# Optimization experiments

Hardware: AMD Instinct MI355X
Metric: run time of the kernel (lower is better)

## Reference

```python
import jax, jax.numpy as jnp
import numpy as np

N = 100000
E = 3200000
H_MLP = 30   # EdgeMLP hidden dim
H_GCN = 10   # GCNEvaluator hidden dim
D_IN = 6     # node_dim + token_dim


def setup_inputs() -> dict:
    key = jax.random.key(0)
    ks = jax.random.split(key, 24)
    s = 0.1
    inp = {
        "x": jax.random.normal(ks[0], (N, 1), jnp.float32),
        "token": jax.random.normal(ks[1], (N, 5), jnp.float32),
        "edge_attr_gen": jax.random.normal(ks[2], (E, 1), jnp.float32),
        "edge_attr_eval": jax.random.uniform(ks[3], (E, 2), jnp.float32),
        "gumbel": jax.random.gumbel(ks[4], (E, 2), jnp.float32),
        "edge_index": jax.random.randint(ks[5], (2, E), 0, N, jnp.int32),
        # EdgeMLP params: Linear(13,30), Linear(30,30), Linear(30,30), Linear(30,2)
        "W0": jax.random.normal(ks[6], (2 * D_IN + 1, H_MLP), jnp.float32) * s,
        "b0": jnp.zeros((H_MLP,), jnp.float32),
        "W1": jax.random.normal(ks[7], (H_MLP, H_MLP), jnp.float32) * s,
        "b1": jnp.zeros((H_MLP,), jnp.float32),
        "W2": jax.random.normal(ks[8], (H_MLP, H_MLP), jnp.float32) * s,
        "b2": jnp.zeros((H_MLP,), jnp.float32),
        "W3": jax.random.normal(ks[9], (H_MLP, 2), jnp.float32) * s,
        "b3": jnp.zeros((2,), jnp.float32),
        # GCNEvaluator params
        "Wl": jax.random.normal(ks[10], (1, 1), jnp.float32) * s,   # edge_weight_lin
        "bl": jnp.zeros((1,), jnp.float32),
        "Wc": jax.random.normal(ks[11], (D_IN, H_GCN), jnp.float32) * s,  # GCNConv weight
        "bc": jnp.zeros((H_GCN,), jnp.float32),
        "Wo": jax.random.normal(ks[12], (H_GCN, 1), jnp.float32) * s,     # output Linear
        "bo": jnp.zeros((1,), jnp.float32),
    }
    return inp


def reference(x, token, edge_attr_gen, edge_attr_eval, gumbel, edge_index,
              W0, b0, W1, b1, W2, b2, W3, b3, Wl, bl, Wc, bc, Wo, bo):
    src = edge_index[0]
    tgt = edge_index[1]
    x_all = jnp.concatenate([x, token], axis=-1)              # [N, 6]

    # ---- generate_graph: edge gather + concat + MLP ----
    ef = jnp.concatenate([x_all[src], x_all[tgt], edge_attr_gen], axis=-1)  # [E, 13]
    h = jax.nn.relu(ef @ W0 + b0)
    h = jax.nn.relu(h @ W1 + b1)
    h = jax.nn.relu(h @ W2 + b2)
    logits = h @ W3 + b3                                      # [E, 2]

    # gumbel_softmax(tau=1.0, hard=True) with straight-through
    y_soft = jax.nn.softmax(logits + gumbel, axis=-1)
    y_hard = jax.nn.one_hot(jnp.argmax(y_soft, axis=-1), 2, dtype=y_soft.dtype)
    y = y_hard + y_soft - jax.lax.stop_gradient(y_soft)
    edge_value = y[:, 1:2]                                    # [E, 1]

    # ---- evaluate_graph: GCNEvaluator ----
    combined = jnp.concatenate([edge_attr_eval, edge_value], axis=-1)  # [E, 3]
    mask = combined[:, -2] * (1.0 - combined[:, -1])
    ew = jax.nn.sigmoid((combined[:, :1] @ Wl + bl)[:, 0]) * mask      # [E]

    # GCNConv(add_self_loops=True, normalize=True)
    loop = jnp.arange(N, dtype=src.dtype)
    row = jnp.concatenate([src, loop])
    col = jnp.concatenate([tgt, loop])
    w = jnp.concatenate([ew, jnp.ones((N,), ew.dtype)])
    deg = jax.ops.segment_sum(w, col, num_segments=N)
    dis = jnp.where(deg > 0, jax.lax.rsqrt(jnp.where(deg > 0, deg, 1.0)), 0.0)
    norm = dis[row] * w * dis[col]
    xw = x_all @ Wc                                            # [N, 10]
    agg = jax.ops.segment_sum(norm[:, None] * xw[row], col, num_segments=N) + bc
    out = jax.nn.sigmoid(agg @ Wo + bo)                        # [N, 1]
    return out
```

## Files before the change

kernel.cpp:

```cpp
#include <hip/hip_runtime.h>

#define NN 100000
#define NE 3200000
#define HM 30
#define HG 10
#define MAXK 26
#define OVF_CAP 8192

__global__ __launch_bounds__(256) void wtrans_kernel(
    const float* __restrict__ W0, const float* __restrict__ W1,
    const float* __restrict__ W2,
    float* __restrict__ W0T, float* __restrict__ W1T, float* __restrict__ W2T)
{
    for (int idx = threadIdx.x; idx < HM * 13; idx += 256) {
        int j = idx / 13, i = idx % 13;
        W0T[j * 16 + i] = W0[i * HM + j];
    }
    for (int idx = threadIdx.x; idx < HM * HM; idx += 256) {
        int j = idx / HM, i = idx % HM;
        W1T[j * 32 + i] = W1[i * HM + j];
        W2T[j * 32 + i] = W2[i * HM + j];
    }
}

__global__ __launch_bounds__(256) void pack_kernel(
    const float* __restrict__ x, const float* __restrict__ token,
    const float* __restrict__ Wc,
    float* __restrict__ xall8, float* __restrict__ xwp)
{
    __shared__ float sWc[6 * HG];
    if (threadIdx.x < 6 * HG) sWc[threadIdx.x] = Wc[threadIdx.x];
    __syncthreads();

    int n = blockIdx.x * 256 + threadIdx.x;
    if (n >= NN) return;

    float xa[6];
    xa[0] = x[n];
    #pragma unroll
    for (int i = 0; i < 5; i++) xa[1 + i] = token[n * 5 + i];

    float4* x4 = (float4*)xall8;
    x4[n * 2 + 0] = make_float4(xa[0], xa[1], xa[2], xa[3]);
    x4[n * 2 + 1] = make_float4(xa[4], xa[5], 0.f, 0.f);

    float w[12];
    #pragma unroll
    for (int k = 0; k < HG; k++) {
        float a = 0.f;
        #pragma unroll
        for (int i = 0; i < 6; i++) a = fmaf(xa[i], sWc[i * HG + k], a);
        w[k] = a;
    }
    w[10] = 0.f; w[11] = 0.f;
    float4* wp = (float4*)(xwp + (size_t)n * 12);
    wp[0] = make_float4(w[0], w[1], w[2], w[3]);
    wp[1] = make_float4(w[4], w[5], w[6], w[7]);
    wp[2] = make_float4(w[8], w[9], w[10], w[11]);
}

__global__ __launch_bounds__(256) void edge_mlp5_kernel(
    const float* __restrict__ xall8,
    const float* __restrict__ eg, const float* __restrict__ ee,
    const float* __restrict__ gum, const int* __restrict__ eidx,
    const float* __restrict__ W0T, const float* __restrict__ b0,
    const float* __restrict__ W1T, const float* __restrict__ b1,
    const float* __restrict__ W2T, const float* __restrict__ b2,
    const float* __restrict__ W3, const float* __restrict__ b3,
    const float* __restrict__ Wl, const float* __restrict__ bl,
    float2* __restrict__ slots, int* __restrict__ cnt,
    int* __restrict__ ohead, int* __restrict__ onxt,
    float* __restrict__ ovf_w, int* __restrict__ ovf_s, int* __restrict__ novf)
{
    int e = blockIdx.x * 256 + threadIdx.x;
    int s = eidx[e];
    int t = eidx[NE + e];

    const float4* x4 = (const float4*)xall8;
    float4 qa = x4[s * 2], qb = x4[s * 2 + 1];
    float4 qc = x4[t * 2], qd = x4[t * 2 + 1];
    float ef[13] = { qa.x, qa.y, qa.z, qa.w, qb.x, qb.y,
                     qc.x, qc.y, qc.z, qc.w, qd.x, qd.y, eg[e] };

    float h[HM], g[HM];
    #pragma unroll
    for (int j = 0; j < HM; j++) {
        float a = b0[j];
        #pragma unroll
        for (int i = 0; i < 13; i++) a = fmaf(ef[i], W0T[j * 16 + i], a);
        h[j] = fmaxf(a, 0.f);
    }
    #pragma unroll
    for (int j = 0; j < HM; j++) {
        float a = b1[j];
        #pragma unroll
        for (int i = 0; i < HM; i++) a = fmaf(h[i], W1T[j * 32 + i], a);
        g[j] = fmaxf(a, 0.f);
    }
    #pragma unroll
    for (int j = 0; j < HM; j++) {
        float a = b2[j];
        #pragma unroll
        for (int i = 0; i < HM; i++) a = fmaf(g[i], W2T[j * 32 + i], a);
        h[j] = fmaxf(a, 0.f);
    }

    float l0 = b3[0], l1 = b3[1];
    #pragma unroll
    for (int i = 0; i < HM; i++) {
        l0 = fmaf(h[i], W3[i * 2 + 0], l0);
        l1 = fmaf(h[i], W3[i * 2 + 1], l1);
    }

    const float2 g2 = ((const float2*)gum)[e];
    float v0 = l0 + g2.x;
    float v1 = l1 + g2.y;

    float ew = 0.f;
    if (!(v1 > v0)) {
        const float2 e2 = ((const float2*)ee)[e];
        float z = fmaf(e2.x, Wl[0], bl[0]);
        ew = e2.y / (1.f + __expf(-z));
    }
    if (ew != 0.f) {
        int slot = atomicAdd(&cnt[t], 1);
        if (slot < MAXK) {
            slots[(size_t)t * MAXK + slot] = make_float2(ew, __int_as_float(s));
        } else {
            int i = atomicAdd(novf, 1);
            if (i < OVF_CAP) {
                ovf_w[i] = ew;
                ovf_s[i] = s;
                onxt[i] = atomicExch(&ohead[t], i);
            }
        }
    }
}

__global__ __launch_bounds__(256) void node_deg_kernel(
    const float2* __restrict__ slots, const int* __restrict__ cnt,
    const int* __restrict__ ohead, const int* __restrict__ onxt,
    const float* __restrict__ ovf_w,
    float* __restrict__ xwp, float* __restrict__ dis)
{
    int n = blockIdx.x * 256 + threadIdx.x;
    if (n >= NN) return;

    int c = cnt[n];
    int cc = c < MAXK ? c : MAXK;
    float deg = 0.f;
    for (int j = 0; j < cc; j++) deg += slots[(size_t)n * MAXK + j].x;
    for (int i = ohead[n]; i >= 0; i = onxt[i]) deg += ovf_w[i];

    float d = rsqrtf(deg + 1.0f);
    dis[n] = d;

    float4* wp = (float4*)(xwp + (size_t)n * 12);
    #pragma unroll
    for (int q = 0; q < 3; q++) {
        float4 v = wp[q];
        v.x *= d; v.y *= d; v.z *= d; v.w *= d;
        wp[q] = v;
    }
}

__global__ __launch_bounds__(256) void gather_out2_kernel(
    const float2* __restrict__ slots, const int* __restrict__ cnt,
    const int* __restrict__ ohead, const int* __restrict__ onxt,
    const float* __restrict__ ovf_w, const int* __restrict__ ovf_s,
    const float* __restrict__ z, const float* __restrict__ dis,
    const float* __restrict__ bc, const float* __restrict__ Wo,
    const float* __restrict__ bo, float* __restrict__ out)
{
    __shared__ float sbc[12], sWo[12], sbo;
    if (threadIdx.x < 12) {
        sbc[threadIdx.x] = (threadIdx.x < HG) ? bc[threadIdx.x] : 0.f;
        sWo[threadIdx.x] = (threadIdx.x < HG) ? Wo[threadIdx.x] : 0.f;
    }
    if (threadIdx.x == 0) sbo = bo[0];
    __syncthreads();

    int n = blockIdx.x * 256 + threadIdx.x;
    if (n >= NN) return;

    const float4* Z = (const float4*)z;
    float4 A0 = make_float4(0.f, 0.f, 0.f, 0.f), A1 = A0, A2 = A0;

    int c = cnt[n];
    int cc = c < MAXK ? c : MAXK;
    for (int j = 0; j < cc; j++) {
        float2 p = slots[(size_t)n * MAXK + j];
        float w = p.x;
        int s = __float_as_int(p.y);
        float4 z0 = Z[s * 3], z1 = Z[s * 3 + 1], z2 = Z[s * 3 + 2];
        A0.x = fmaf(w, z0.x, A0.x); A0.y = fmaf(w, z0.y, A0.y);
        A0.z = fmaf(w, z0.z, A0.z); A0.w = fmaf(w, z0.w, A0.w);
        A1.x = fmaf(w, z1.x, A1.x); A1.y = fmaf(w, z1.y, A1.y);
        A1.z = fmaf(w, z1.z, A1.z); A1.w = fmaf(w, z1.w, A1.w);
        A2.x = fmaf(w, z2.x, A2.x); A2.y = fmaf(w, z2.y, A2.y);
    }
    for (int i = ohead[n]; i >= 0; i = onxt[i]) {
        float w = ovf_w[i];
        int s = ovf_s[i];
        float4 z0 = Z[s * 3], z1 = Z[s * 3 + 1], z2 = Z[s * 3 + 2];
        A0.x = fmaf(w, z0.x, A0.x); A0.y = fmaf(w, z0.y, A0.y);
        A0.z = fmaf(w, z0.z, A0.z); A0.w = fmaf(w, z0.w, A0.w);
        A1.x = fmaf(w, z1.x, A1.x); A1.y = fmaf(w, z1.y, A1.y);
        A1.z = fmaf(w, z1.z, A1.z); A1.w = fmaf(w, z1.w, A1.w);
        A2.x = fmaf(w, z2.x, A2.x); A2.y = fmaf(w, z2.y, A2.y);
    }

    float4 s0 = Z[n * 3], s1 = Z[n * 3 + 1], s2 = Z[n * 3 + 2];
    A0.x += s0.x; A0.y += s0.y; A0.z += s0.z; A0.w += s0.w;
    A1.x += s1.x; A1.y += s1.y; A1.z += s1.z; A1.w += s1.w;
    A2.x += s2.x; A2.y += s2.y;

    float d = dis[n];
    float v[10] = { A0.x, A0.y, A0.z, A0.w, A1.x, A1.y, A1.z, A1.w, A2.x, A2.y };
    float o = sbo;
    #pragma unroll
    for (int k = 0; k < HG; k++)
        o = fmaf(fmaf(v[k], d, sbc[k]), sWo[k], o);
    out[n] = 1.f / (1.f + __expf(-o));
}

__global__ __launch_bounds__(256) void edge_mlp_kernel(
    const float* __restrict__ x, const float* __restrict__ token,
    const float* __restrict__ eg, const float* __restrict__ ee,
    const float* __restrict__ gum, const int* __restrict__ eidx,
    const float* __restrict__ W0, const float* __restrict__ b0,
    const float* __restrict__ W1, const float* __restrict__ b1,
    const float* __restrict__ W2, const float* __restrict__ b2,
    const float* __restrict__ W3, const float* __restrict__ b3,
    const float* __restrict__ Wl, const float* __restrict__ bl,
    float* __restrict__ ew_out, float* __restrict__ deg)
{
    __shared__ float sW0[13 * HM];
    __shared__ float sW1[HM * HM];
    __shared__ float sW2[HM * HM];
    __shared__ float sW3f[HM * 2];
    __shared__ float sb0[HM], sb1[HM], sb2[HM], sb3[2];
    __shared__ float sWl, sbl;

    for (int i = threadIdx.x; i < 13 * HM; i += 256) sW0[i] = W0[i];
    for (int i = threadIdx.x; i < HM * HM; i += 256) sW1[i] = W1[i];
    for (int i = threadIdx.x; i < HM * HM; i += 256) sW2[i] = W2[i];
    for (int i = threadIdx.x; i < HM * 2; i += 256) sW3f[i] = W3[i];
    if (threadIdx.x < HM) {
        sb0[threadIdx.x] = b0[threadIdx.x];
        sb1[threadIdx.x] = b1[threadIdx.x];
        sb2[threadIdx.x] = b2[threadIdx.x];
    }
    if (threadIdx.x < 2) sb3[threadIdx.x] = b3[threadIdx.x];
    if (threadIdx.x == 0) { sWl = Wl[0]; sbl = bl[0]; }
    __syncthreads();

    int e = blockIdx.x * 256 + threadIdx.x;
    if (e >= NE) return;
    int s = eidx[e];
    int t = eidx[NE + e];

    float ef[13];
    ef[0] = x[s];
    #pragma unroll
    for (int i = 0; i < 5; i++) ef[1 + i] = token[s * 5 + i];
    ef[6] = x[t];
    #pragma unroll
    for (int i = 0; i < 5; i++) ef[7 + i] = token[t * 5 + i];
    ef[12] = eg[e];

    float h[HM], h2[HM];
    #pragma unroll
    for (int j = 0; j < HM; j++) {
        float a = sb0[j];
        #pragma unroll
        for (int i = 0; i < 13; i++) a = fmaf(ef[i], sW0[i * HM + j], a);
        h[j] = a > 0.f ? a : 0.f;
    }
    #pragma unroll
    for (int j = 0; j < HM; j++) {
        float a = sb1[j];
        #pragma unroll
        for (int i = 0; i < HM; i++) a = fmaf(h[i], sW1[i * HM + j], a);
        h2[j] = a > 0.f ? a : 0.f;
    }
    #pragma unroll
    for (int j = 0; j < HM; j++) {
        float a = sb2[j];
        #pragma unroll
        for (int i = 0; i < HM; i++) a = fmaf(h2[i], sW2[i * HM + j], a);
        h[j] = a > 0.f ? a : 0.f;
    }
    float l0 = sb3[0], l1 = sb3[1];
    #pragma unroll
    for (int i = 0; i < HM; i++) {
        l0 = fmaf(h[i], sW3f[i * 2 + 0], l0);
        l1 = fmaf(h[i], sW3f[i * 2 + 1], l1);
    }
    const float2 g2 = ((const float2*)gum)[e];
    float v0 = l0 + g2.x, v1 = l1 + g2.y;
    float ew = 0.f;
    if (!(v1 > v0)) {
        const float2 ee2 = ((const float2*)ee)[e];
        float z = fmaf(ee2.x, sWl, sbl);
        ew = ee2.y / (1.f + __expf(-z));
    }
    ew_out[e] = ew;
    if (ew != 0.f) atomicAdd(&deg[t], ew);
}

__global__ __launch_bounds__(256) void node_pre_kernel(
    const float* __restrict__ x, const float* __restrict__ token,
    const float* __restrict__ Wc, const float* __restrict__ deg,
    float* __restrict__ xw, float* __restrict__ dis)
{
    __shared__ float sWc[6 * HG];
    if (threadIdx.x < 6 * HG) sWc[threadIdx.x] = Wc[threadIdx.x];
    __syncthreads();
    int n = blockIdx.x * 256 + threadIdx.x;
    if (n >= NN) return;
    float xa[6];
    xa[0] = x[n];
    #pragma unroll
    for (int i = 0; i < 5; i++) xa[1 + i] = token[n * 5 + i];
    #pragma unroll
    for (int k = 0; k < HG; k++) {
        float a = 0.f;
        #pragma unroll
        for (int i = 0; i < 6; i++) a = fmaf(xa[i], sWc[i * HG + k], a);
        xw[n * HG + k] = a;
    }
    dis[n] = rsqrtf(deg[n] + 1.0f);
}

__global__ __launch_bounds__(256) void edge_scatter_kernel(
    const int* __restrict__ eidx, const float* __restrict__ ew,
    const float* __restrict__ dis, const float* __restrict__ xw,
    float* __restrict__ agg)
{
    int e = blockIdx.x * 256 + threadIdx.x;
    if (e >= NE) return;
    float w = ew[e];
    if (w == 0.f) return;
    int s = eidx[e];
    int t = eidx[NE + e];
    float norm = dis[s] * w * dis[t];
    #pragma unroll
    for (int k = 0; k < HG; k++)
        atomicAdd(&agg[t * HG + k], norm * xw[s * HG + k]);
}

__global__ __launch_bounds__(256) void node_out_kernel(
    const float* __restrict__ agg, const float* __restrict__ xw,
    const float* __restrict__ dis, const float* __restrict__ bc,
    const float* __restrict__ Wo, const float* __restrict__ bo,
    float* __restrict__ out)
{
    __shared__ float sbc[HG], sWo[HG], sbo;
    if (threadIdx.x < HG) { sbc[threadIdx.x] = bc[threadIdx.x]; sWo[threadIdx.x] = Wo[threadIdx.x]; }
    if (threadIdx.x == 0) sbo = bo[0];
    __syncthreads();
    int n = blockIdx.x * 256 + threadIdx.x;
    if (n >= NN) return;
    float d = dis[n];
    float self = d * d;
    float acc = sbo;
    #pragma unroll
    for (int k = 0; k < HG; k++) {
        float v = agg[n * HG + k] + xw[n * HG + k] * self + sbc[k];
        acc = fmaf(v, sWo[k], acc);
    }
    out[n] = 1.f / (1.f + __expf(-acc));
}

extern "C" void kernel_launch(void* const* d_in, const int* in_sizes, int n_in,
                              void* d_out, int out_size, void* d_ws, size_t ws_size,
                              hipStream_t stream) {
    const float* x   = (const float*)d_in[0];
    const float* tok = (const float*)d_in[1];
    const float* eg  = (const float*)d_in[2];
    const float* ee  = (const float*)d_in[3];
    const float* gum = (const float*)d_in[4];
    const int*   ei  = (const int*)d_in[5];
    const float* W0  = (const float*)d_in[6];
    const float* b0  = (const float*)d_in[7];
    const float* W1  = (const float*)d_in[8];
    const float* b1  = (const float*)d_in[9];
    const float* W2  = (const float*)d_in[10];
    const float* b2  = (const float*)d_in[11];
    const float* W3  = (const float*)d_in[12];
    const float* b3  = (const float*)d_in[13];
    const float* Wl  = (const float*)d_in[14];
    const float* bl  = (const float*)d_in[15];
    const float* Wc  = (const float*)d_in[16];
    const float* bc  = (const float*)d_in[17];
    const float* Wo  = (const float*)d_in[18];
    const float* bo  = (const float*)d_in[19];
    float* out = (float*)d_out;

    dim3 blk(256);
    dim3 egrid(NE / 256);
    dim3 ngrid((NN + 255) / 256);

    size_t off_xall8 = 0;
    size_t off_xwp   = off_xall8 + (size_t)NN * 8;
    size_t off_slots = off_xwp + (size_t)NN * 12;
    size_t off_cnt   = off_slots + (size_t)NN * MAXK * 2;
    size_t off_novf  = off_cnt + NN;
    size_t off_dis   = off_novf + 1;
    size_t off_ohead = off_dis + NN;
    size_t off_ovfw  = off_ohead + NN;
    size_t off_ovfs  = off_ovfw + OVF_CAP;
    size_t off_onxt  = off_ovfs + OVF_CAP;
    size_t off_w0t   = (off_onxt + OVF_CAP + 15) & ~(size_t)15;
    size_t off_w1t   = off_w0t + 30 * 16;
    size_t off_w2t   = off_w1t + 30 * 32;
    size_t need_new  = (off_w2t + 30 * 32) * sizeof(float);

    if (ws_size >= need_new) {
        float*  ws    = (float*)d_ws;
        float*  xall8 = ws + off_xall8;
        float*  xwp   = ws + off_xwp;
        float2* slots = (float2*)(ws + off_slots);
        int*    cnt   = (int*)(ws + off_cnt);
        int*    novf  = (int*)(ws + off_novf);
        float*  dis   = ws + off_dis;
        int*    ohead = (int*)(ws + off_ohead);
        float*  ovf_w = ws + off_ovfw;
        int*    ovf_s = (int*)(ws + off_ovfs);
        int*    onxt  = (int*)(ws + off_onxt);
        float*  W0T   = ws + off_w0t;
        float*  W1T   = ws + off_w1t;
        float*  W2T   = ws + off_w2t;

        hipMemsetAsync(cnt, 0, (size_t)(NN + 1) * sizeof(int), stream);
        hipMemsetAsync(ohead, 0xFF, (size_t)NN * sizeof(int), stream);

        wtrans_kernel<<<dim3(1), blk, 0, stream>>>(W0, W1, W2, W0T, W1T, W2T);
        pack_kernel<<<ngrid, blk, 0, stream>>>(x, tok, Wc, xall8, xwp);
        edge_mlp5_kernel<<<egrid, blk, 0, stream>>>(xall8, eg, ee, gum, ei,
                                                    W0T, b0, W1T, b1, W2T, b2,
                                                    W3, b3, Wl, bl, slots, cnt,
                                                    ohead, onxt, ovf_w, ovf_s, novf);
        node_deg_kernel<<<ngrid, blk, 0, stream>>>(slots, cnt, ohead, onxt, ovf_w,
                                                   xwp, dis);
        gather_out2_kernel<<<ngrid, blk, 0, stream>>>(slots, cnt, ohead, onxt,
                                                      ovf_w, ovf_s, xwp, dis,
                                                      bc, Wo, bo, out);
    } else {
        float* ws  = (float*)d_ws;
        float* ew  = ws;
        float* deg = ew + NE;
        float* agg = deg + NN;
        float* xw  = agg + (size_t)NN * HG;
        float* dis = xw + (size_t)NN * HG;

        hipMemsetAsync(deg, 0, (size_t)(NN + (size_t)NN * HG) * sizeof(float), stream);
        edge_mlp_kernel<<<egrid, blk, 0, stream>>>(x, tok, eg, ee, gum, ei,
                                                   W0, b0, W1, b1, W2, b2, W3, b3,
                                                   Wl, bl, ew, deg);
        node_pre_kernel<<<ngrid, blk, 0, stream>>>(x, tok, Wc, deg, xw, dis);
        edge_scatter_kernel<<<egrid, blk, 0, stream>>>(ei, ew, dis, xw, agg);
        node_out_kernel<<<ngrid, blk, 0, stream>>>(agg, xw, dis, bc, Wo, bo, out);
    }
}
```

Baseline: 415.1 us.

## Use packed FMA in edge MLP, atomic degree, 4-lane per-node gather

The edge MLP now uses two-wide packed FMAs over zero-padded transposed weights, and its launch bounds gain a minimum-blocks hint. It also accumulates node degree with a float atomic, so the degree kernel shrinks to an rsqrt pass and the separate prescaling of xw is dropped. The gather now scales each neighbour's contribution by dis[s] on the fly and splits every node's slot list across four lanes, combined with xor shuffles. The aim is to cut FP32 instruction count and the long per-node serial gather loops, at the cost of an extra atomic per kept edge and an additional dis lookup per neighbour.

```diff
diff --git a/kernel.cpp b/kernel.cpp
--- a/kernel.cpp
+++ b/kernel.cpp
@@ -7,19 +7,31 @@
 #define MAXK 26
 #define OVF_CAP 8192
 
+typedef float __attribute__((ext_vector_type(2))) f32x2;
+
+__device__ __forceinline__ f32x2 pkfma(f32x2 a, f32x2 b, f32x2 c) {
+#if __has_builtin(__builtin_elementwise_fma)
+    return __builtin_elementwise_fma(a, b, c);
+#else
+    f32x2 r; r.x = fmaf(a.x, b.x, c.x); r.y = fmaf(a.y, b.y, c.y); return r;
+#endif
+}
+
 __global__ __launch_bounds__(256) void wtrans_kernel(
     const float* __restrict__ W0, const float* __restrict__ W1,
     const float* __restrict__ W2,
     float* __restrict__ W0T, float* __restrict__ W1T, float* __restrict__ W2T)
 {
-    for (int idx = threadIdx.x; idx < HM * 13; idx += 256) {
-        int j = idx / 13, i = idx % 13;
-        W0T[j * 16 + i] = W0[i * HM + j];
-    }
-    for (int idx = threadIdx.x; idx < HM * HM; idx += 256) {
-        int j = idx / HM, i = idx % HM;
-        W1T[j * 32 + i] = W1[i * HM + j];
-        W2T[j * 32 + i] = W2[i * HM + j];
+    for (int idx = threadIdx.x; idx < HM * 16; idx += 256) {
+        int j = idx >> 4, i = idx & 15;
+        W0T[idx] = (i < 13) ? W0[i * HM + j] : 0.f;
+    }
+    for (int idx = threadIdx.x; idx < HM * 32; idx += 256) {
+        int j = idx >> 5, i = idx & 31;
+        float v1 = (i < HM) ? W1[i * HM + j] : 0.f;
+        float v2 = (i < HM) ? W2[i * HM + j] : 0.f;
+        W1T[idx] = v1;
+        W2T[idx] = v2;
     }
 }
 
@@ -59,7 +71,7 @@
     wp[2] = make_float4(w[8], w[9], w[10], w[11]);
 }
 
-__global__ __launch_bounds__(256) void edge_mlp5_kernel(
+__global__ __launch_bounds__(256, 2) void edge_mlp6_kernel(
     const float* __restrict__ xall8,
     const float* __restrict__ eg, const float* __restrict__ ee,
     const float* __restrict__ gum, const int* __restrict__ eidx,
@@ -68,7 +80,7 @@
     const float* __restrict__ W2T, const float* __restrict__ b2,
     const float* __restrict__ W3, const float* __restrict__ b3,
     const float* __restrict__ Wl, const float* __restrict__ bl,
-    float2* __restrict__ slots, int* __restrict__ cnt,
+    float2* __restrict__ slots, int* __restrict__ cnt, float* __restrict__ deg,
     int* __restrict__ ohead, int* __restrict__ onxt,
     float* __restrict__ ovf_w, int* __restrict__ ovf_s, int* __restrict__ novf)
 {
@@ -79,30 +91,52 @@
     const float4* x4 = (const float4*)xall8;
     float4 qa = x4[s * 2], qb = x4[s * 2 + 1];
     float4 qc = x4[t * 2], qd = x4[t * 2 + 1];
-    float ef[13] = { qa.x, qa.y, qa.z, qa.w, qb.x, qb.y,
-                     qc.x, qc.y, qc.z, qc.w, qd.x, qd.y, eg[e] };
+
+    f32x2 ef2[7];
+    ef2[0] = f32x2{ qa.x, qa.y };
+    ef2[1] = f32x2{ qa.z, qa.w };
+    ef2[2] = f32x2{ qb.x, qb.y };
+    ef2[3] = f32x2{ qc.x, qc.y };
+    ef2[4] = f32x2{ qc.z, qc.w };
+    ef2[5] = f32x2{ qd.x, qd.y };
+    ef2[6] = f32x2{ eg[e], 0.f };
 
     float h[HM], g[HM];
+
     #pragma unroll
     for (int j = 0; j < HM; j++) {
-        float a = b0[j];
-        #pragma unroll
-        for (int i = 0; i < 13; i++) a = fmaf(ef[i], W0T[j * 16 + i], a);
-        h[j] = fmaxf(a, 0.f);
-    }
-    #pragma unroll
-    for (int j = 0; j < HM; j++) {
-        float a = b1[j];
-        #pragma unroll
-        for (int i = 0; i < HM; i++) a = fmaf(h[i], W1T[j * 32 + i], a);
-        g[j] = fmaxf(a, 0.f);
-    }
-    #pragma unroll
-    for (int j = 0; j < HM; j++) {
-        float a = b2[j];
-        #pragma unroll
-        for (int i = 0; i < HM; i++) a = fmaf(g[i], W2T[j * 32 + i], a);
-        h[j] = fmaxf(a, 0.f);
+        const f32x2* w2 = (const f32x2*)(W0T + j * 16);
+        f32x2 a2 = f32x2{ b0[j], 0.f };
+        #pragma unroll
+        for (int p = 0; p < 7; p++) a2 = pkfma(ef2[p], w2[p], a2);
+        h[j] = fmaxf(a2.x + a2.y, 0.f);
+    }
+
+    {
+        f32x2 hp[15];
+        #pragma unroll
+        for (int p = 0; p < 15; p++) hp[p] = f32x2{ h[2 * p], h[2 * p + 1] };
+        #pragma unroll
+        for (int j = 0; j < HM; j++) {
+            const f32x2* w2 = (const f32x2*)(W1T + j * 32);
+            f32x2 a2 = f32x2{ b1[j], 0.f };
+            #pragma unroll
+            for (int p = 0; p < 15; p++) a2 = pkfma(hp[p], w2[p], a2);
+            g[j] = fmaxf(a2.x + a2.y, 0.f);
+        }
+    }
+    {
+        f32x2 gp[15];
+        #pragma unroll
+        for (int p = 0; p < 15; p++) gp[p] = f32x2{ g[2 * p], g[2 * p + 1] };
+        #pragma unroll
+        for (int j = 0; j < HM; j++) {
+            const f32x2* w2 = (const f32x2*)(W2T + j * 32);
+            f32x2 a2 = f32x2{ b2[j], 0.f };
+            #pragma unroll
+            for (int p = 0; p < 15; p++) a2 = pkfma(gp[p], w2[p], a2);
+            h[j] = fmaxf(a2.x + a2.y, 0.f);
+        }
     }
 
     float l0 = b3[0], l1 = b3[1];
@@ -123,6 +157,7 @@
         ew = e2.y / (1.f + __expf(-z));
     }
     if (ew != 0.f) {
+        atomicAdd(&deg[t], ew);
         int slot = atomicAdd(&cnt[t], 1);
         if (slot < MAXK) {
             slots[(size_t)t * MAXK + slot] = make_float2(ew, __int_as_float(s));
@@ -137,38 +172,19 @@
     }
 }
 
-__global__ __launch_bounds__(256) void node_deg_kernel(
-    const float2* __restrict__ slots, const int* __restrict__ cnt,
-    const int* __restrict__ ohead, const int* __restrict__ onxt,
-    const float* __restrict__ ovf_w,
-    float* __restrict__ xwp, float* __restrict__ dis)
+__global__ __launch_bounds__(256) void node_dis_kernel(
+    const float* __restrict__ deg, float* __restrict__ dis)
 {
     int n = blockIdx.x * 256 + threadIdx.x;
     if (n >= NN) return;
-
-    int c = cnt[n];
-    int cc = c < MAXK ? c : MAXK;
-    float deg = 0.f;
-    for (int j = 0; j < cc; j++) deg += slots[(size_t)n * MAXK + j].x;
-    for (int i = ohead[n]; i >= 0; i = onxt[i]) deg += ovf_w[i];
-
-    float d = rsqrtf(deg + 1.0f);
-    dis[n] = d;
-
-    float4* wp = (float4*)(xwp + (size_t)n * 12);
-    #pragma unroll
-    for (int q = 0; q < 3; q++) {
-        float4 v = wp[q];
-        v.x *= d; v.y *= d; v.z *= d; v.w *= d;
-        wp[q] = v;
-    }
-}
-
-__global__ __launch_bounds__(256) void gather_out2_kernel(
+    dis[n] = rsqrtf(deg[n] + 1.0f);
+}
+
+__global__ __launch_bounds__(256) void gather_out3_kernel(
     const float2* __restrict__ slots, const int* __restrict__ cnt,
     const int* __restrict__ ohead, const int* __restrict__ onxt,
     const float* __restrict__ ovf_w, const int* __restrict__ ovf_s,
-    const float* __restrict__ z, const float* __restrict__ dis,
+    const float* __restrict__ xwp, const float* __restrict__ dis,
     const float* __restrict__ bc, const float* __restrict__ Wo,
     const float* __restrict__ bo, float* __restrict__ out)
 {
@@ -180,18 +196,20 @@
     if (threadIdx.x == 0) sbo = bo[0];
     __syncthreads();
 
-    int n = blockIdx.x * 256 + threadIdx.x;
+    int tg = blockIdx.x * 256 + threadIdx.x;
+    int n = tg >> 2;
+    int k = tg & 3;
     if (n >= NN) return;
 
-    const float4* Z = (const float4*)z;
+    const float4* Z = (const float4*)xwp;
     float4 A0 = make_float4(0.f, 0.f, 0.f, 0.f), A1 = A0, A2 = A0;
 
     int c = cnt[n];
     int cc = c < MAXK ? c : MAXK;
-    for (int j = 0; j < cc; j++) {
+    for (int j = k; j < cc; j += 4) {
         float2 p = slots[(size_t)n * MAXK + j];
-        float w = p.x;
         int s = __float_as_int(p.y);
+        float w = p.x * dis[s];
         float4 z0 = Z[s * 3], z1 = Z[s * 3 + 1], z2 = Z[s * 3 + 2];
         A0.x = fmaf(w, z0.x, A0.x); A0.y = fmaf(w, z0.y, A0.y);
         A0.z = fmaf(w, z0.z, A0.z); A0.w = fmaf(w, z0.w, A0.w);
@@ -199,29 +217,41 @@
         A1.z = fmaf(w, z1.z, A1.z); A1.w = fmaf(w, z1.w, A1.w);
         A2.x = fmaf(w, z2.x, A2.x); A2.y = fmaf(w, z2.y, A2.y);
     }
-    for (int i = ohead[n]; i >= 0; i = onxt[i]) {
-        float w = ovf_w[i];
-        int s = ovf_s[i];
-        float4 z0 = Z[s * 3], z1 = Z[s * 3 + 1], z2 = Z[s * 3 + 2];
-        A0.x = fmaf(w, z0.x, A0.x); A0.y = fmaf(w, z0.y, A0.y);
-        A0.z = fmaf(w, z0.z, A0.z); A0.w = fmaf(w, z0.w, A0.w);
-        A1.x = fmaf(w, z1.x, A1.x); A1.y = fmaf(w, z1.y, A1.y);
-        A1.z = fmaf(w, z1.z, A1.z); A1.w = fmaf(w, z1.w, A1.w);
-        A2.x = fmaf(w, z2.x, A2.x); A2.y = fmaf(w, z2.y, A2.y);
-    }
-
-    float4 s0 = Z[n * 3], s1 = Z[n * 3 + 1], s2 = Z[n * 3 + 2];
-    A0.x += s0.x; A0.y += s0.y; A0.z += s0.z; A0.w += s0.w;
-    A1.x += s1.x; A1.y += s1.y; A1.z += s1.z; A1.w += s1.w;
-    A2.x += s2.x; A2.y += s2.y;
-
-    float d = dis[n];
+    if (k == 0) {
+        for (int i = ohead[n]; i >= 0; i = onxt[i]) {
+            int s = ovf_s[i];
+            float w = ovf_w[i] * dis[s];
+            float4 z0 = Z[s * 3], z1 = Z[s * 3 + 1], z2 = Z[s * 3 + 2];
+            A0.x = fmaf(w, z0.x, A0.x); A0.y = fmaf(w, z0.y, A0.y);
+            A0.z = fmaf(w, z0.z, A0.z); A0.w = fmaf(w, z0.w, A0.w);
+            A1.x = fmaf(w, z1.x, A1.x); A1.y = fmaf(w, z1.y, A1.y);
+            A1.z = fmaf(w, z1.z, A1.z); A1.w = fmaf(w, z1.w, A1.w);
+            A2.x = fmaf(w, z2.x, A2.x); A2.y = fmaf(w, z2.y, A2.y);
+        }
+        float wn = dis[n];
+        float4 s0 = Z[n * 3], s1 = Z[n * 3 + 1], s2 = Z[n * 3 + 2];
+        A0.x = fmaf(wn, s0.x, A0.x); A0.y = fmaf(wn, s0.y, A0.y);
+        A0.z = fmaf(wn, s0.z, A0.z); A0.w = fmaf(wn, s0.w, A0.w);
+        A1.x = fmaf(wn, s1.x, A1.x); A1.y = fmaf(wn, s1.y, A1.y);
+        A1.z = fmaf(wn, s1.z, A1.z); A1.w = fmaf(wn, s1.w, A1.w);
+        A2.x = fmaf(wn, s2.x, A2.x); A2.y = fmaf(wn, s2.y, A2.y);
+    }
+
     float v[10] = { A0.x, A0.y, A0.z, A0.w, A1.x, A1.y, A1.z, A1.w, A2.x, A2.y };
-    float o = sbo;
-    #pragma unroll
-    for (int k = 0; k < HG; k++)
-        o = fmaf(fmaf(v[k], d, sbc[k]), sWo[k], o);
-    out[n] = 1.f / (1.f + __expf(-o));
+    #pragma unroll
+    for (int q = 0; q < 10; q++) {
+        v[q] += __shfl_xor(v[q], 1);
+        v[q] += __shfl_xor(v[q], 2);
+    }
+
+    if (k == 0) {
+        float d = dis[n];
+        float o = sbo;
+        #pragma unroll
+        for (int q = 0; q < HG; q++)
+            o = fmaf(fmaf(v[q], d, sbc[q]), sWo[q], o);
+        out[n] = 1.f / (1.f + __expf(-o));
+    }
 }
 
 __global__ __launch_bounds__(256) void edge_mlp_kernel(
@@ -401,13 +431,15 @@
     dim3 blk(256);
     dim3 egrid(NE / 256);
     dim3 ngrid((NN + 255) / 256);
+    dim3 g4grid((NN * 4 + 255) / 256);
 
     size_t off_xall8 = 0;
     size_t off_xwp   = off_xall8 + (size_t)NN * 8;
     size_t off_slots = off_xwp + (size_t)NN * 12;
     size_t off_cnt   = off_slots + (size_t)NN * MAXK * 2;
     size_t off_novf  = off_cnt + NN;
-    size_t off_dis   = off_novf + 1;
+    size_t off_deg   = off_novf + 1;
+    size_t off_dis   = off_deg + NN;
     size_t off_ohead = off_dis + NN;
     size_t off_ovfw  = off_ohead + NN;
     size_t off_ovfs  = off_ovfw + OVF_CAP;
@@ -424,6 +456,7 @@
         float2* slots = (float2*)(ws + off_slots);
         int*    cnt   = (int*)(ws + off_cnt);
         int*    novf  = (int*)(ws + off_novf);
+        float*  deg   = ws + off_deg;
         float*  dis   = ws + off_dis;
         int*    ohead = (int*)(ws + off_ohead);
         float*  ovf_w = ws + off_ovfw;
@@ -433,20 +466,19 @@
         float*  W1T   = ws + off_w1t;
         float*  W2T   = ws + off_w2t;
 
-        hipMemsetAsync(cnt, 0, (size_t)(NN + 1) * sizeof(int), stream);
+        hipMemsetAsync(cnt, 0, (size_t)(2 * NN + 1) * sizeof(int), stream);
         hipMemsetAsync(ohead, 0xFF, (size_t)NN * sizeof(int), stream);
 
         wtrans_kernel<<<dim3(1), blk, 0, stream>>>(W0, W1, W2, W0T, W1T, W2T);
         pack_kernel<<<ngrid, blk, 0, stream>>>(x, tok, Wc, xall8, xwp);
-        edge_mlp5_kernel<<<egrid, blk, 0, stream>>>(xall8, eg, ee, gum, ei,
+        edge_mlp6_kernel<<<egrid, blk, 0, stream>>>(xall8, eg, ee, gum, ei,
                                                     W0T, b0, W1T, b1, W2T, b2,
-                                                    W3, b3, Wl, bl, slots, cnt,
+                                                    W3, b3, Wl, bl, slots, cnt, deg,
                                                     ohead, onxt, ovf_w, ovf_s, novf);
-        node_deg_kernel<<<ngrid, blk, 0, stream>>>(slots, cnt, ohead, onxt, ovf_w,
-                                                   xwp, dis);
-        gather_out2_kernel<<<ngrid, blk, 0, stream>>>(slots, cnt, ohead, onxt,
-                                                      ovf_w, ovf_s, xwp, dis,
-                                                      bc, Wo, bo, out);
+        node_dis_kernel<<<ngrid, blk, 0, stream>>>(deg, dis);
+        gather_out3_kernel<<<g4grid, blk, 0, stream>>>(slots, cnt, ohead, onxt,
+                                                       ovf_w, ovf_s, xwp, dis,
+                                                       bc, Wo, bo, out);
     } else {
         float* ws  = (float*)d_ws;
         float* ew  = ws;
```

Result: faster. 396.8 us (-4.4%).
